# Optimization experiments

Hardware: AMD Instinct MI355X
Metric: run time of the kernel (lower is better)

The kernel has to match this reference:

```python
import jax, jax.numpy as jnp
import numpy as np


def _l2norm(x, eps=1e-12):
    # F.normalize(p=2, dim=-1): x / max(||x||_2, eps)
    n = jnp.linalg.norm(x, axis=-1, keepdims=True)
    return x / jnp.maximum(n, eps)


def _dwconv3x3(x, w):
    # depthwise 3x3 conv, padding=1, no bias. x: [B,C,H,W], w: [C,1,3,3]
    return jax.lax.conv_general_dilated(
        x, w, window_strides=(1, 1), padding='SAME',
        feature_group_count=x.shape[1],
        dimension_numbers=('NCHW', 'OIHW', 'NCHW'))


def setup_inputs() -> dict:
    key = jax.random.key(0)
    ks = jax.random.split(key, 10)
    B, H, W, C = 2, 256, 256, 64
    heads, dh, dim_out = 8, 64, 64
    hd = heads * dh  # 512
    s = 0.02
    return {
        'x_in': jax.random.normal(ks[0], (B, H, W, C), jnp.float32),
        'Wq': jax.random.normal(ks[1], (C, hd), jnp.float32) * s,
        'Wk': jax.random.normal(ks[2], (C, hd), jnp.float32) * s,
        'Wv': jax.random.normal(ks[3], (C, hd), jnp.float32) * s,
        'rescale': jnp.ones((heads, 1, 1), jnp.float32),
        'Wproj': jax.random.normal(ks[4], (hd, dim_out), jnp.float32) * s,
        'bproj': jnp.zeros((dim_out,), jnp.float32),
        'Wc1d': jax.random.normal(ks[5], (hd, dim_out), jnp.float32) * s,
        'bc1d': jnp.zeros((dim_out,), jnp.float32),
        'Wpe1': jax.random.normal(ks[6], (dim_out, 1, 3, 3), jnp.float32) * s,
        'Wpe2': jax.random.normal(ks[7], (dim_out, 1, 3, 3), jnp.float32) * s,
    }


def reference(x_in, Wq, Wk, Wv, rescale, Wproj, bproj, Wc1d, bc1d, Wpe1, Wpe2):
    b, h, w, c = x_in.shape
    heads = rescale.shape[0]
    hd = Wq.shape[1]
    dh = hd // heads
    dim_out = Wproj.shape[1]
    ds = 2

    # AvgPool2d(2,2) on channels-last input
    xp = x_in.reshape(b, h // ds, ds, w // ds, ds, c).mean(axis=(2, 4))
    n_ds = (h // ds) * (w // ds)
    xd = xp.reshape(b, n_ds, c)

    # q,k from downsampled tokens; v from full-res tokens
    q = (xd @ Wq).reshape(b, n_ds, heads, dh).transpose(0, 2, 3, 1)   # [b,heads,dh,n_ds]
    k = (xd @ Wk).reshape(b, n_ds, heads, dh).transpose(0, 2, 3, 1)   # [b,heads,dh,n_ds]
    v_inp = x_in.reshape(b, h * w, c) @ Wv                             # [b,n,hd]
    v = v_inp.reshape(b, h * w, heads, dh).transpose(0, 2, 3, 1)       # [b,heads,dh,n]

    q = _l2norm(q)
    k = _l2norm(k)

    # channel (transposed) attention: [b,heads,dh,dh]
    attn = jnp.einsum('bhin,bhjn->bhij', k, q) * rescale
    attn = jax.nn.softmax(attn, axis=-1)

    xa = jnp.einsum('bhij,bhjn->bhin', attn, v)                        # [b,heads,dh,n]
    xa = xa.transpose(0, 3, 1, 2).reshape(b, h * w, hd)                # [b,n,hd]
    out_c = (xa @ Wproj + bproj).reshape(b, h, w, dim_out)

    # positional branch: 1x1 conv (pointwise) then two depthwise 3x3 convs with GELU
    p = v_inp @ Wc1d + bc1d                                            # [b,n,dim_out]
    p = p.reshape(b, h, w, dim_out).transpose(0, 3, 1, 2)              # [b,dim_out,h,w]
    p = _dwconv3x3(p, Wpe1)
    p = jax.nn.gelu(p, approximate=False)
    p = _dwconv3x3(p, Wpe2)
    out_p = p.transpose(0, 2, 3, 1)                                    # [b,h,w,dim_out]

    return out_c + out_p
```

## Files before the change

### kernel.cpp

```cpp
#include <hip/hip_runtime.h>
#include <math.h>


typedef unsigned short u16;
typedef unsigned int u32;
typedef __attribute__((ext_vector_type(8))) short short8;
typedef __attribute__((ext_vector_type(4))) float f32x4;

__device__ __forceinline__ float bf2f(u16 h) { return __uint_as_float(((u32)h) << 16); }
__device__ __forceinline__ u16 f2bf(float f) {
    u32 u = __float_as_uint(f);
    return (u16)((u + 0x7fffu + ((u >> 16) & 1u)) >> 16);
}
__device__ __forceinline__ float rbf(float f) { return bf2f(f2bf(f)); }
__device__ __forceinline__ u32 pk2(float lo, float hi) {
    return (u32)f2bf(lo) | ((u32)f2bf(hi) << 16);
}
__device__ __forceinline__ void unpack8(uint4 v, float* f) {
    u32 a[4] = {v.x, v.y, v.z, v.w};
#pragma unroll
    for (int i = 0; i < 4; ++i) {
        f[2 * i]     = __uint_as_float(a[i] << 16);
        f[2 * i + 1] = __uint_as_float(a[i] & 0xffff0000u);
    }
}
__device__ __forceinline__ float gelu_exact(float v) {
    return 0.5f * v * (1.f + erff(v * 0.70710678118654752f));
}

__global__ __launch_bounds__(256) void k_front(
    const float* __restrict__ x,
    const float* __restrict__ wq_f, const float* __restrict__ wk_f,
    const float* __restrict__ wv_f, const float* __restrict__ rs_f,
    const float* __restrict__ wp_f, const float* __restrict__ bp_f,
    const float* __restrict__ wc_f, const float* __restrict__ bc_f,
    const float* __restrict__ p1_f, const float* __restrict__ p2_f,
    u32* __restrict__ wb32, float* __restrict__ Wpos,
    u16* __restrict__ xb, float* __restrict__ partials) {
    __shared__ float xvs[64 * 68];
    int blk = blockIdx.x;
    int t = threadIdx.x;
    if (blk < 323) {
        u32 pid = (u32)blk * 256u + t;
        if (pid < 82564u) {
            const float* src; u32 p;
            if      (pid < 16384u) { src = wq_f; p = pid; }
            else if (pid < 32768u) { src = wk_f; p = pid - 16384u; }
            else if (pid < 49152u) { src = wv_f; p = pid - 32768u; }
            else if (pid < 49156u) { src = rs_f; p = pid - 49152u; }
            else if (pid < 65540u) { src = wp_f; p = pid - 49156u; }
            else if (pid < 65572u) { src = bp_f; p = pid - 65540u; }
            else if (pid < 81956u) { src = wc_f; p = pid - 65572u; }
            else if (pid < 81988u) { src = bc_f; p = pid - 81956u; }
            else if (pid < 82276u) { src = p1_f; p = pid - 81988u; }
            else                   { src = p2_f; p = pid - 82276u; }
            wb32[pid] = (u32)f2bf(src[2 * p]) | ((u32)f2bf(src[2 * p + 1]) << 16);
        }
    } else if (blk < 387) {
        int c = blk - 323;
        int o = t & 63, ch = t >> 6;
        const float* wvr = wv_f + c * 512 + ch * 128;
        const float* wcr = wc_f + (size_t)(ch * 128) * 64 + o;
        float s = 0.f;
        for (int kk = 0; kk < 128; ++kk)
            s += rbf(wvr[kk]) * rbf(wcr[(size_t)kk * 64]);
        xvs[ch * 64 + o] = s;
        __syncthreads();
        if (t < 64)
            Wpos[c * 64 + t] = (xvs[t] + xvs[64 + t]) + (xvs[128 + t] + xvs[192 + t]);
    } else {
        int gb = blk - 387;
        int b = gb >> 8, sub = gb & 255;
        int py = sub >> 1, half = sub & 1;
        const size_t rowbase = (size_t)(b * 256 + 2 * py) * 16384 + (size_t)half * 8192;
#pragma unroll
        for (int i2 = 0; i2 < 4; ++i2) {
            int u = t + 256 * i2;
            int P = u >> 4, cq = u & 15;
            size_t o0 = rowbase + (size_t)(2 * P) * 64 + cq * 4;
            float4 a0 = *(const float4*)(x + o0);
            float4 a1 = *(const float4*)(x + o0 + 64);
            float4 a2 = *(const float4*)(x + o0 + 16384);
            float4 a3 = *(const float4*)(x + o0 + 16384 + 64);
            *(uint2*)(xb + o0)              = make_uint2(pk2(a0.x, a0.y), pk2(a0.z, a0.w));
            *(uint2*)(xb + o0 + 64)         = make_uint2(pk2(a1.x, a1.y), pk2(a1.z, a1.w));
            *(uint2*)(xb + o0 + 16384)      = make_uint2(pk2(a2.x, a2.y), pk2(a2.z, a2.w));
            *(uint2*)(xb + o0 + 16384 + 64) = make_uint2(pk2(a3.x, a3.y), pk2(a3.z, a3.w));
            float4 s;
            s.x = 0.25f * (a0.x + a1.x + a2.x + a3.x);
            s.y = 0.25f * (a0.y + a1.y + a2.y + a3.y);
            s.z = 0.25f * (a0.z + a1.z + a2.z + a3.z);
            s.w = 0.25f * (a0.w + a1.w + a2.w + a3.w);
            *(float4*)(&xvs[P * 68 + cq * 4]) = s;
        }
        __syncthreads();
        int r0 = (t >> 4) << 2, c0 = (t & 15) << 2;
        float acc[4][4] = {{0.f}};
        for (int P = 0; P < 64; ++P) {
            float4 av = *(const float4*)(&xvs[P * 68 + r0]);
            float4 bv = *(const float4*)(&xvs[P * 68 + c0]);
            float ar[4] = {av.x, av.y, av.z, av.w};
            float br[4] = {bv.x, bv.y, bv.z, bv.w};
#pragma unroll
            for (int i = 0; i < 4; ++i)
#pragma unroll
                for (int j = 0; j < 4; ++j)
                    acc[i][j] += ar[i] * br[j];
        }
        float* outp = partials + (size_t)gb * 4096;
#pragma unroll
        for (int i = 0; i < 4; ++i)
            *(float4*)(&outp[(r0 + i) * 64 + c0]) =
                make_float4(acc[i][0], acc[i][1], acc[i][2], acc[i][3]);
    }
}

__global__ __launch_bounds__(256) void k_mid1(
    const float* __restrict__ partials, float* __restrict__ G4, float* __restrict__ Weff,
    const u16* __restrict__ xb, const float* __restrict__ Wpos,
    const u16* __restrict__ bc1d, u16* __restrict__ pbuf) {
    __shared__ u16 sm[128 * 72];
    int blk = blockIdx.x;
    int t = threadIdx.x;
    if (blk < 128) {
        int gid = blk * 256 + t;
        int e = gid & 4095, ch = (gid >> 12) & 3, b = gid >> 14;
        const float* p0 = partials + ((size_t)(b * 256 + ch * 64)) * 4096 + e;
        float s = 0.f;
        for (int p = 0; p < 64; ++p)
            s += p0[(size_t)p * 4096];
        G4[gid] = s;
        if (gid < 8192) Weff[gid] = 0.f;
        return;
    }
    int pb = blk - 128;
    int lane = t & 63, wv = t >> 6;
    int col = lane & 15, quad = lane >> 4;

    short8 bf[2][4];
#pragma unroll
    for (int kh = 0; kh < 2; ++kh)
#pragma unroll
        for (int nt = 0; nt < 4; ++nt) {
            short8 v;
#pragma unroll
            for (int j = 0; j < 8; ++j)
                v[j] = (short)f2bf(Wpos[(kh * 32 + quad * 8 + j) * 64 + nt * 16 + col]);
            bf[kh][nt] = v;
        }
    float bias[4];
#pragma unroll
    for (int nt = 0; nt < 4; ++nt) bias[nt] = bf2f(bc1d[nt * 16 + col]);

    size_t base = (size_t)pb * 128;
#pragma unroll
    for (int g = 0; g < 2; ++g) {
        int P0 = wv * 32 + g * 16;
        const short8* ap = (const short8*)(xb + (base + P0 + col) * 64);
        short8 a0 = ap[quad];
        short8 a1 = ap[4 + quad];
#pragma unroll
        for (int nt = 0; nt < 4; ++nt) {
            f32x4 acc = {0.f, 0.f, 0.f, 0.f};
            acc = __builtin_amdgcn_mfma_f32_16x16x32_bf16(a0, bf[0][nt], acc, 0, 0, 0);
            acc = __builtin_amdgcn_mfma_f32_16x16x32_bf16(a1, bf[1][nt], acc, 0, 0, 0);
#pragma unroll
            for (int r = 0; r < 4; ++r)
                sm[(P0 + quad * 4 + r) * 72 + nt * 16 + col] = f2bf(acc[r] + bias[nt]);
        }
    }
    __syncthreads();
#pragma unroll
    for (int k = 0; k < 4; ++k) {
        int linear = k * 256 + t;
        int px = linear >> 3, oct = linear & 7;
        uint4 v = *(const uint4*)(&sm[px * 72 + oct * 8]);
        *(uint4*)(pbuf + (base + px) * 64 + oct * 8) = v;
    }
}

__global__ __launch_bounds__(256) void k_gwqk_norms(
    const float* __restrict__ G4, const u16* __restrict__ wqb, const u16* __restrict__ wkb,
    float* __restrict__ T, float* __restrict__ nq, float* __restrict__ nk) {
    __shared__ __align__(16) float Gs[64 * 68];
    __shared__ __align__(16) float Ps[64 * 68];
    int blk = blockIdx.x, t = threadIdx.x;
    int b = blk >> 4, sel = (blk >> 3) & 1, jg = blk & 7;
    const u16* Wsel = sel ? wkb : wqb;
    {
        int base = t * 16;
        int row = base >> 6, col = base & 63;
        const float* Gb = G4 + (size_t)b * 16384;
#pragma unroll
        for (int q = 0; q < 4; ++q) {
            float4 g0 = *(const float4*)(&Gb[base + 4 * q]);
            float4 g1 = *(const float4*)(&Gb[4096 + base + 4 * q]);
            float4 g2 = *(const float4*)(&Gb[8192 + base + 4 * q]);
            float4 g3 = *(const float4*)(&Gb[12288 + base + 4 * q]);
            *(float4*)(&Gs[row * 68 + col + 4 * q]) = make_float4(
                (g0.x + g1.x) + (g2.x + g3.x), (g0.y + g1.y) + (g2.y + g3.y),
                (g0.z + g1.z) + (g2.z + g3.z), (g0.w + g1.w) + (g2.w + g3.w));
        }
    }
    __syncthreads();
    int c = t >> 2, jq = t & 3;
    int jbase = jg * 64 + jq * 16;
    float Tr[16];
#pragma unroll
    for (int jj = 0; jj < 16; ++jj) Tr[jj] = 0.f;
    for (int k = 0; k < 64; ++k) {
        short8 w0 = *(const short8*)(&Wsel[k * 512 + jbase]);
        short8 w1 = *(const short8*)(&Wsel[k * 512 + jbase + 8]);
        float g = Gs[c * 68 + k];
#pragma unroll
        for (int jj = 0; jj < 8; ++jj) {
            Tr[jj]     += g * bf2f((u16)w0[jj]);
            Tr[8 + jj] += g * bf2f((u16)w1[jj]);
        }
    }
    if (sel == 0) {
#pragma unroll
        for (int q = 0; q < 4; ++q)
            *(float4*)(&T[(size_t)(b * 64 + c) * 512 + jbase + 4 * q]) =
                make_float4(Tr[4 * q], Tr[4 * q + 1], Tr[4 * q + 2], Tr[4 * q + 3]);
    }
    {
        short8 wc0 = *(const short8*)(&Wsel[c * 512 + jbase]);
        short8 wc1 = *(const short8*)(&Wsel[c * 512 + jbase + 8]);
#pragma unroll
        for (int jj = 0; jj < 8; ++jj) {
            Ps[c * 68 + jq * 16 + jj]     = bf2f((u16)wc0[jj]) * Tr[jj];
            Ps[c * 68 + jq * 16 + 8 + jj] = bf2f((u16)wc1[jj]) * Tr[8 + jj];
        }
    }
    __syncthreads();
    if (t < 64) {
        float s = 0.f;
        for (int cc = 0; cc < 64; ++cc) s += Ps[cc * 68 + t];
        float n = fmaxf(sqrtf(fmaxf(s, 0.f)), 1e-12f);
        (sel ? nk : nq)[b * 512 + jg * 64 + t] = n;
    }
}

__global__ __launch_bounds__(256) void k_mid2(
    const u16* __restrict__ wkb, const u16* __restrict__ wpb, const u16* __restrict__ wvb,
    const u16* __restrict__ rsb,
    const float* __restrict__ T, const float* __restrict__ nq, const float* __restrict__ nk,
    float* __restrict__ Weff,
    const u16* __restrict__ pbuf, const u16* __restrict__ wpe1, u16* __restrict__ tbuf) {
    __shared__ __align__(16) char shm[53248];
    int blk = blockIdx.x, t = threadIdx.x;
    if (blk < 16) {
        float* Ts    = (float*)shm;
        float* attns = (float*)(shm + 17408);
        u16*   Wks   = (u16*)(shm + 34816);
        u16*   Wpjs  = (u16*)(shm + 44032);
        float* Pls = Ts;
        u16*   Wvs = Wks;
        int b = blk >> 3, h = blk & 7;
        {
            int c = t >> 2, j0 = (t & 3) * 16;
#pragma unroll
            for (int q = 0; q < 4; ++q)
                *(float4*)(&Ts[c * 68 + j0 + 4 * q]) =
                    *(const float4*)(&T[(size_t)(b * 64 + c) * 512 + h * 64 + j0 + 4 * q]);
            *(short8*)(&Wks[c * 72 + j0])     = *(const short8*)(&wkb[c * 512 + h * 64 + j0]);
            *(short8*)(&Wks[c * 72 + j0 + 8]) = *(const short8*)(&wkb[c * 512 + h * 64 + j0 + 8]);
            *(short8*)(&Wpjs[c * 72 + j0])     = *(const short8*)(&wpb[(h * 64 + c) * 64 + j0]);
            *(short8*)(&Wpjs[c * 72 + j0 + 8]) = *(const short8*)(&wpb[(h * 64 + c) * 64 + j0 + 8]);
        }
        __syncthreads();
        {
            int i = t >> 2, jq = t & 3;
            float L[16];
#pragma unroll
            for (int jj = 0; jj < 16; ++jj) L[jj] = 0.f;
            for (int c = 0; c < 64; ++c) {
                float wk = bf2f(Wks[c * 72 + i]);
#pragma unroll
                for (int q = 0; q < 4; ++q) {
                    float4 tv = *(const float4*)(&Ts[c * 68 + jq * 16 + 4 * q]);
                    L[4 * q + 0] += wk * tv.x;
                    L[4 * q + 1] += wk * tv.y;
                    L[4 * q + 2] += wk * tv.z;
                    L[4 * q + 3] += wk * tv.w;
                }
            }
            float rs = bf2f(rsb[h]);
            float nki = nk[b * 512 + h * 64 + i];
            float nqv[16];
#pragma unroll
            for (int q = 0; q < 4; ++q) {
                float4 nv = *(const float4*)(&nq[b * 512 + h * 64 + jq * 16 + 4 * q]);
                nqv[4 * q] = nv.x; nqv[4 * q + 1] = nv.y;
                nqv[4 * q + 2] = nv.z; nqv[4 * q + 3] = nv.w;
            }
            float m = -1e30f;
#pragma unroll
            for (int jj = 0; jj < 16; ++jj) {
                L[jj] = L[jj] * rs / (nki * nqv[jj]);
                m = fmaxf(m, L[jj]);
            }
            m = fmaxf(m, __shfl_xor(m, 1));
            m = fmaxf(m, __shfl_xor(m, 2));
            float s = 0.f;
#pragma unroll
            for (int jj = 0; jj < 16; ++jj) {
                L[jj] = __expf(L[jj] - m);
                s += L[jj];
            }
            s += __shfl_xor(s, 1);
            s += __shfl_xor(s, 2);
            float inv = 1.f / s;
#pragma unroll
            for (int q = 0; q < 4; ++q)
                *(float4*)(&attns[i * 68 + jq * 16 + 4 * q]) =
                    make_float4(L[4 * q] * inv, L[4 * q + 1] * inv,
                                L[4 * q + 2] * inv, L[4 * q + 3] * inv);
        }
        __syncthreads();
        {
            int c = t >> 2, j0 = (t & 3) * 16;
            *(short8*)(&Wvs[c * 72 + j0])     = *(const short8*)(&wvb[c * 512 + h * 64 + j0]);
            *(short8*)(&Wvs[c * 72 + j0 + 8]) = *(const short8*)(&wvb[c * 512 + h * 64 + j0 + 8]);
            int j = t >> 2, oq = t & 3;
            float Pl[16];
#pragma unroll
            for (int jj = 0; jj < 16; ++jj) Pl[jj] = 0.f;
            for (int i2 = 0; i2 < 64; ++i2) {
                float a = attns[i2 * 68 + j];
                short8 w0 = *(const short8*)(&Wpjs[i2 * 72 + oq * 16]);
                short8 w1 = *(const short8*)(&Wpjs[i2 * 72 + oq * 16 + 8]);
#pragma unroll
                for (int jj = 0; jj < 8; ++jj) {
                    Pl[jj]     += a * bf2f((u16)w0[jj]);
                    Pl[8 + jj] += a * bf2f((u16)w1[jj]);
                }
            }
#pragma unroll
            for (int q = 0; q < 4; ++q)
                *(float4*)(&Pls[j * 68 + oq * 16 + 4 * q]) =
                    make_float4(Pl[4 * q], Pl[4 * q + 1], Pl[4 * q + 2], Pl[4 * q + 3]);
        }
        __syncthreads();
        {
            int c = t >> 2, oq = t & 3;
            float acc[16];
#pragma unroll
            for (int jj = 0; jj < 16; ++jj) acc[jj] = 0.f;
            for (int j2 = 0; j2 < 64; ++j2) {
                float wv = bf2f(Wvs[c * 72 + j2]);
#pragma unroll
                for (int q = 0; q < 4; ++q) {
                    float4 pv = *(const float4*)(&Pls[j2 * 68 + oq * 16 + 4 * q]);
                    acc[4 * q + 0] += wv * pv.x;
                    acc[4 * q + 1] += wv * pv.y;
                    acc[4 * q + 2] += wv * pv.z;
                    acc[4 * q + 3] += wv * pv.w;
                }
            }
            float* W = Weff + b * 4096 + c * 64 + oq * 16;
#pragma unroll
            for (int jj = 0; jj < 16; ++jj) atomicAdd(&W[jj], acc[jj]);
        }
        return;
    }
    u16* sm = (u16*)shm;
    int cb = blk - 16;
    int b  = cb >> 9;
    int ty = (cb >> 3) & 63;
    int tx = cb & 7;
    int gy0 = ty * 4, gx0 = tx * 32;

    for (int i = t; i < 1632; i += 256) {
        int px = i >> 3, ch = i & 7;
        int hy = px / 34, hx = px - hy * 34;
        int gy = gy0 + hy - 1, gx = gx0 + hx - 1;
        uint4 v = make_uint4(0, 0, 0, 0);
        if ((unsigned)gy < 256u && (unsigned)gx < 256u)
            v = *(const uint4*)(pbuf + ((size_t)((b << 16) + (gy << 8) + gx)) * 64 + ch * 8);
        *(uint4*)(&sm[px * 72 + ch * 8]) = v;
    }
    int oct = t & 7;
    float w[8][9];
#pragma unroll
    for (int j = 0; j < 8; ++j)
#pragma unroll
        for (int k = 0; k < 9; ++k) w[j][k] = bf2f(wpe1[(oct * 8 + j) * 9 + k]);
    __syncthreads();

#pragma unroll
    for (int s = 0; s < 4; ++s) {
        int lp = (t >> 3) + s * 32;
        int ly = lp >> 5, lx = lp & 31;
        float acc[8] = {0.f, 0.f, 0.f, 0.f, 0.f, 0.f, 0.f, 0.f};
#pragma unroll
        for (int dy = 0; dy < 3; ++dy)
#pragma unroll
            for (int dx = 0; dx < 3; ++dx) {
                int hp = (ly + dy) * 34 + lx + dx;
                uint4 v = *(const uint4*)(&sm[hp * 72 + oct * 8]);
                float f[8];
                unpack8(v, f);
                int tap = dy * 3 + dx;
#pragma unroll
                for (int j = 0; j < 8; ++j) acc[j] += f[j] * w[j][tap];
            }
        u32 pk[4];
#pragma unroll
        for (int q = 0; q < 4; ++q)
            pk[q] = pk2(gelu_exact(acc[2 * q]), gelu_exact(acc[2 * q + 1]));
        size_t gpix = (size_t)(b << 16) + ((size_t)(gy0 + ly) << 8) + gx0 + lx;
        *(uint4*)(tbuf + gpix * 64 + oct * 8) = make_uint4(pk[0], pk[1], pk[2], pk[3]);
    }
}

__global__ __launch_bounds__(256) void k_final(const u16* __restrict__ xb,
                                               const u16* __restrict__ tbuf,
                                               const float* __restrict__ Weff,
                                               const u16* __restrict__ wpe2,
                                               const u16* __restrict__ bproj,
                                               float* __restrict__ out) {
    __shared__ u16 sm[204 * 72];
    __shared__ float stage[128 * 68];
    int t = threadIdx.x;
    int blk = blockIdx.x;
    int b  = blk >> 9;
    int ty = (blk >> 3) & 63;
    int tx = blk & 7;
    int gy0 = ty * 4, gx0 = tx * 32;

    for (int i = t; i < 1632; i += 256) {
        int px = i >> 3, ch = i & 7;
        int hy = px / 34, hx = px - hy * 34;
        int gy = gy0 + hy - 1, gx = gx0 + hx - 1;
        uint4 v = make_uint4(0, 0, 0, 0);
        if ((unsigned)gy < 256u && (unsigned)gx < 256u)
            v = *(const uint4*)(tbuf + ((size_t)((b << 16) + (gy << 8) + gx)) * 64 + ch * 8);
        *(uint4*)(&sm[px * 72 + ch * 8]) = v;
    }
    int oct = t & 7;
    {
        float w[8][9];
#pragma unroll
        for (int j = 0; j < 8; ++j)
#pragma unroll
            for (int k = 0; k < 9; ++k) w[j][k] = bf2f(wpe2[(oct * 8 + j) * 9 + k]);
        __syncthreads();
#pragma unroll
        for (int s = 0; s < 4; ++s) {
            int lp = (t >> 3) + s * 32;
            int ly = lp >> 5, lx = lp & 31;
            float acc[8] = {0.f, 0.f, 0.f, 0.f, 0.f, 0.f, 0.f, 0.f};
#pragma unroll
            for (int dy = 0; dy < 3; ++dy)
#pragma unroll
                for (int dx = 0; dx < 3; ++dx) {
                    int hp = (ly + dy) * 34 + lx + dx;
                    uint4 v = *(const uint4*)(&sm[hp * 72 + oct * 8]);
                    float f[8];
                    unpack8(v, f);
                    int tap = dy * 3 + dx;
#pragma unroll
                    for (int j = 0; j < 8; ++j) acc[j] += f[j] * w[j][tap];
                }
#pragma unroll
            for (int j = 0; j < 8; ++j)
                stage[lp * 68 + oct * 8 + j] = acc[j];
        }
    }
    __syncthreads();

    int lane = t & 63, wv = t >> 6;
    int col = lane & 15, quad = lane >> 4;
    const float* W = Weff + b * 4096;
    short8 bf[2][4];
#pragma unroll
    for (int kh = 0; kh < 2; ++kh)
#pragma unroll
        for (int nt = 0; nt < 4; ++nt) {
            short8 v;
#pragma unroll
            for (int j = 0; j < 8; ++j)
                v[j] = (short)f2bf(W[(kh * 32 + quad * 8 + j) * 64 + nt * 16 + col]);
            bf[kh][nt] = v;
        }
    float bias[4];
#pragma unroll
    for (int nt = 0; nt < 4; ++nt) bias[nt] = bf2f(bproj[nt * 16 + col]);

#pragma unroll
    for (int g = 0; g < 2; ++g) {
        int grp = wv * 2 + g;
        int ly = grp >> 1;
        int lxb = (grp & 1) * 16;
        size_t rowpix = (size_t)(b << 16) + ((size_t)(gy0 + ly) << 8) + gx0;
        const short8* ap = (const short8*)(xb + (rowpix + lxb + col) * 64);
        short8 a0 = ap[quad];
        short8 a1 = ap[4 + quad];
#pragma unroll
        for (int nt = 0; nt < 4; ++nt) {
            f32x4 acc = {0.f, 0.f, 0.f, 0.f};
            acc = __builtin_amdgcn_mfma_f32_16x16x32_bf16(a0, bf[0][nt], acc, 0, 0, 0);
            acc = __builtin_amdgcn_mfma_f32_16x16x32_bf16(a1, bf[1][nt], acc, 0, 0, 0);
#pragma unroll
            for (int r = 0; r < 4; ++r) {
                int lp = ly * 32 + lxb + quad * 4 + r;
                stage[lp * 68 + nt * 16 + col] += acc[r] + bias[nt];
            }
        }
    }
    __syncthreads();

#pragma unroll
    for (int k = 0; k < 8; ++k) {
        int linear = k * 256 + t;
        int px = linear >> 4, c4 = linear & 15;
        int ly = px >> 5, lx = px & 31;
        float4 v = *(const float4*)(&stage[px * 68 + c4 * 4]);
        size_t gpix = (size_t)(b << 16) + ((size_t)(gy0 + ly) << 8) + gx0 + lx;
        *(float4*)(out + gpix * 64 + c4 * 4) = v;
    }
}

extern "C" void kernel_launch(void* const* d_in, const int* in_sizes, int n_in,
                              void* d_out, int out_size, void* d_ws, size_t ws_size,
                              hipStream_t stream) {
    const float* x = (const float*)d_in[0];
    float* out = (float*)d_out;

    char* w = (char*)d_ws;
    size_t off = 0;
    auto alloc = [&](size_t bytes) -> void* {
        void* p = w + off;
        off += (bytes + 255) & ~(size_t)255;
        return p;
    };
    u16* xb = (u16*)alloc((size_t)16777216 * 2);
    u16* wb = (u16*)alloc((size_t)165128 * 2);
    u16* wqb = wb;
    u16* wkb = wqb + 32768;
    u16* wvb = wkb + 32768;
    u16* rsb = wvb + 32768;
    u16* wpb = rsb + 8;
    u16* bpb = wpb + 32768;
    u16* wcb = bpb + 64;
    u16* bcb = wcb + 32768;
    u16* p1b = bcb + 64;
    u16* p2b = p1b + 576;
    (void)wcb;

    float* partials = (float*)alloc((size_t)512 * 4096 * 4);
    float* G4       = (float*)alloc((size_t)2 * 4 * 4096 * 4);
    float* T        = (float*)alloc((size_t)2 * 64 * 512 * 4);
    float* nq       = (float*)alloc((size_t)2 * 512 * 4);
    float* nk       = (float*)alloc((size_t)2 * 512 * 4);
    float* Weff     = (float*)alloc((size_t)2 * 4096 * 4);
    float* Wpos     = (float*)alloc((size_t)4096 * 4);
    u16*   pbuf     = (u16*)alloc((size_t)2 * 65536 * 64 * 2);
    u16*   tbuf     = (u16*)alloc((size_t)2 * 65536 * 64 * 2);

    hipLaunchKernelGGL(k_front, dim3(899), dim3(256), 0, stream,
                       x,
                       (const float*)d_in[1], (const float*)d_in[2], (const float*)d_in[3],
                       (const float*)d_in[4], (const float*)d_in[5], (const float*)d_in[6],
                       (const float*)d_in[7], (const float*)d_in[8], (const float*)d_in[9],
                       (const float*)d_in[10],
                       (u32*)wb, Wpos, xb, partials);
    hipLaunchKernelGGL(k_mid1, dim3(1152), dim3(256), 0, stream,
                       partials, G4, Weff, xb, Wpos, bcb, pbuf);
    hipLaunchKernelGGL(k_gwqk_norms, dim3(32), dim3(256), 0, stream,
                       G4, wqb, wkb, T, nq, nk);
    hipLaunchKernelGGL(k_mid2, dim3(1040), dim3(256), 0, stream,
                       wkb, wpb, wvb, rsb, T, nq, nk, Weff, pbuf, p1b, tbuf);
    hipLaunchKernelGGL(k_final, dim3(1024), dim3(256), 0, stream,
                       xb, tbuf, Weff, p2b, bpb, out);
}
```

Before: 166.9 us.

## Fuse Gram-weight product and norm kernel into attention mid-stage blocks

Removes the separate k_gwqk_norms launch and computes the G·Wq/G·Wk products and the q/k norms directly inside the 16 attention blocks of k_mid2, keeping T and the norms in shared memory rather than in global buffers. This saves one kernel launch and a global round-trip for T, nq and nk. In exchange each attention block does more serial work: two 64x64x64 products plus reductions with extra barriers, and Wk is now read from global memory inside the logits loop instead of from shared memory. That lengthens the critical path of the 16 heavy blocks that run alongside the conv blocks.

New measurement: 174.0 us. +4.3%, slower.

```diff
diff --git a/kernel.cpp b/kernel.cpp
--- a/kernel.cpp
+++ b/kernel.cpp
@@ -179,107 +179,115 @@
     }
 }
 
-__global__ __launch_bounds__(256) void k_gwqk_norms(
-    const float* __restrict__ G4, const u16* __restrict__ wqb, const u16* __restrict__ wkb,
-    float* __restrict__ T, float* __restrict__ nq, float* __restrict__ nk) {
-    __shared__ __align__(16) float Gs[64 * 68];
-    __shared__ __align__(16) float Ps[64 * 68];
-    int blk = blockIdx.x, t = threadIdx.x;
-    int b = blk >> 4, sel = (blk >> 3) & 1, jg = blk & 7;
-    const u16* Wsel = sel ? wkb : wqb;
-    {
-        int base = t * 16;
-        int row = base >> 6, col = base & 63;
-        const float* Gb = G4 + (size_t)b * 16384;
-#pragma unroll
-        for (int q = 0; q < 4; ++q) {
-            float4 g0 = *(const float4*)(&Gb[base + 4 * q]);
-            float4 g1 = *(const float4*)(&Gb[4096 + base + 4 * q]);
-            float4 g2 = *(const float4*)(&Gb[8192 + base + 4 * q]);
-            float4 g3 = *(const float4*)(&Gb[12288 + base + 4 * q]);
-            *(float4*)(&Gs[row * 68 + col + 4 * q]) = make_float4(
-                (g0.x + g1.x) + (g2.x + g3.x), (g0.y + g1.y) + (g2.y + g3.y),
-                (g0.z + g1.z) + (g2.z + g3.z), (g0.w + g1.w) + (g2.w + g3.w));
-        }
-    }
-    __syncthreads();
-    int c = t >> 2, jq = t & 3;
-    int jbase = jg * 64 + jq * 16;
-    float Tr[16];
-#pragma unroll
-    for (int jj = 0; jj < 16; ++jj) Tr[jj] = 0.f;
-    for (int k = 0; k < 64; ++k) {
-        short8 w0 = *(const short8*)(&Wsel[k * 512 + jbase]);
-        short8 w1 = *(const short8*)(&Wsel[k * 512 + jbase + 8]);
-        float g = Gs[c * 68 + k];
-#pragma unroll
-        for (int jj = 0; jj < 8; ++jj) {
-            Tr[jj]     += g * bf2f((u16)w0[jj]);
-            Tr[8 + jj] += g * bf2f((u16)w1[jj]);
-        }
-    }
-    if (sel == 0) {
-#pragma unroll
-        for (int q = 0; q < 4; ++q)
-            *(float4*)(&T[(size_t)(b * 64 + c) * 512 + jbase + 4 * q]) =
-                make_float4(Tr[4 * q], Tr[4 * q + 1], Tr[4 * q + 2], Tr[4 * q + 3]);
-    }
-    {
-        short8 wc0 = *(const short8*)(&Wsel[c * 512 + jbase]);
-        short8 wc1 = *(const short8*)(&Wsel[c * 512 + jbase + 8]);
-#pragma unroll
-        for (int jj = 0; jj < 8; ++jj) {
-            Ps[c * 68 + jq * 16 + jj]     = bf2f((u16)wc0[jj]) * Tr[jj];
-            Ps[c * 68 + jq * 16 + 8 + jj] = bf2f((u16)wc1[jj]) * Tr[8 + jj];
-        }
-    }
-    __syncthreads();
-    if (t < 64) {
-        float s = 0.f;
-        for (int cc = 0; cc < 64; ++cc) s += Ps[cc * 68 + t];
-        float n = fmaxf(sqrtf(fmaxf(s, 0.f)), 1e-12f);
-        (sel ? nk : nq)[b * 512 + jg * 64 + t] = n;
-    }
-}
-
 __global__ __launch_bounds__(256) void k_mid2(
-    const u16* __restrict__ wkb, const u16* __restrict__ wpb, const u16* __restrict__ wvb,
+    const u16* __restrict__ wkb, const u16* __restrict__ wqb,
+    const u16* __restrict__ wpb, const u16* __restrict__ wvb,
     const u16* __restrict__ rsb,
-    const float* __restrict__ T, const float* __restrict__ nq, const float* __restrict__ nk,
-    float* __restrict__ Weff,
+    const float* __restrict__ G4, float* __restrict__ Weff,
     const u16* __restrict__ pbuf, const u16* __restrict__ wpe1, u16* __restrict__ tbuf) {
     __shared__ __align__(16) char shm[53248];
     int blk = blockIdx.x, t = threadIdx.x;
     if (blk < 16) {
-        float* Ts    = (float*)shm;
-        float* attns = (float*)(shm + 17408);
-        u16*   Wks   = (u16*)(shm + 34816);
-        u16*   Wpjs  = (u16*)(shm + 44032);
-        float* Pls = Ts;
-        u16*   Wvs = Wks;
+        float* Ts   = (float*)shm;
+        float* Ps   = (float*)(shm + 17408);
+        float* Gs   = (float*)(shm + 34816);
+        u16*   Wpjs = (u16*)(shm + 34816);
+        u16*   Wvs  = (u16*)(shm + 34816 + 9216);
+        float* attns = Ps;
+        float* Pls   = Ts;
         int b = blk >> 3, h = blk & 7;
-        {
-            int c = t >> 2, j0 = (t & 3) * 16;
+        int c = t >> 2, jq = t & 3, j0 = jq * 16;
+        {
+            int base = t * 16;
+            int row = base >> 6, col = base & 63;
+            const float* Gb = G4 + (size_t)b * 16384;
+#pragma unroll
+            for (int q = 0; q < 4; ++q) {
+                float4 g0 = *(const float4*)(&Gb[base + 4 * q]);
+                float4 g1 = *(const float4*)(&Gb[4096 + base + 4 * q]);
+                float4 g2 = *(const float4*)(&Gb[8192 + base + 4 * q]);
+                float4 g3 = *(const float4*)(&Gb[12288 + base + 4 * q]);
+                *(float4*)(&Gs[row * 68 + col + 4 * q]) = make_float4(
+                    (g0.x + g1.x) + (g2.x + g3.x), (g0.y + g1.y) + (g2.y + g3.y),
+                    (g0.z + g1.z) + (g2.z + g3.z), (g0.w + g1.w) + (g2.w + g3.w));
+            }
+        }
+        __syncthreads();
+        float Tr[16];
+        {
+#pragma unroll
+            for (int jj = 0; jj < 16; ++jj) Tr[jj] = 0.f;
+            for (int k = 0; k < 64; ++k) {
+                short8 w0 = *(const short8*)(&wkb[k * 512 + h * 64 + j0]);
+                short8 w1 = *(const short8*)(&wkb[k * 512 + h * 64 + j0 + 8]);
+                float g = Gs[c * 68 + k];
+#pragma unroll
+                for (int jj = 0; jj < 8; ++jj) {
+                    Tr[jj]     += g * bf2f((u16)w0[jj]);
+                    Tr[8 + jj] += g * bf2f((u16)w1[jj]);
+                }
+            }
+            short8 wc0 = *(const short8*)(&wkb[c * 512 + h * 64 + j0]);
+            short8 wc1 = *(const short8*)(&wkb[c * 512 + h * 64 + j0 + 8]);
+#pragma unroll
+            for (int jj = 0; jj < 8; ++jj) {
+                Ps[c * 68 + j0 + jj]     = bf2f((u16)wc0[jj]) * Tr[jj];
+                Ps[c * 68 + j0 + 8 + jj] = bf2f((u16)wc1[jj]) * Tr[8 + jj];
+            }
+        }
+        __syncthreads();
+        if (t < 64) {
+            float s = 0.f;
+            for (int cc = 0; cc < 64; ++cc) s += Ps[cc * 68 + t];
+            Ts[t * 68 + 64] = fmaxf(sqrtf(fmaxf(s, 0.f)), 1e-12f);
+        }
+        {
+#pragma unroll
+            for (int jj = 0; jj < 16; ++jj) Tr[jj] = 0.f;
+            for (int k = 0; k < 64; ++k) {
+                short8 w0 = *(const short8*)(&wqb[k * 512 + h * 64 + j0]);
+                short8 w1 = *(const short8*)(&wqb[k * 512 + h * 64 + j0 + 8]);
+                float g = Gs[c * 68 + k];
+#pragma unroll
+                for (int jj = 0; jj < 8; ++jj) {
+                    Tr[jj]     += g * bf2f((u16)w0[jj]);
+                    Tr[8 + jj] += g * bf2f((u16)w1[jj]);
+                }
+            }
 #pragma unroll
             for (int q = 0; q < 4; ++q)
                 *(float4*)(&Ts[c * 68 + j0 + 4 * q]) =
-                    *(const float4*)(&T[(size_t)(b * 64 + c) * 512 + h * 64 + j0 + 4 * q]);
-            *(short8*)(&Wks[c * 72 + j0])     = *(const short8*)(&wkb[c * 512 + h * 64 + j0]);
-            *(short8*)(&Wks[c * 72 + j0 + 8]) = *(const short8*)(&wkb[c * 512 + h * 64 + j0 + 8]);
+                    make_float4(Tr[4 * q], Tr[4 * q + 1], Tr[4 * q + 2], Tr[4 * q + 3]);
+        }
+        __syncthreads();
+        {
+            short8 wc0 = *(const short8*)(&wqb[c * 512 + h * 64 + j0]);
+            short8 wc1 = *(const short8*)(&wqb[c * 512 + h * 64 + j0 + 8]);
+#pragma unroll
+            for (int jj = 0; jj < 8; ++jj) {
+                Ps[c * 68 + j0 + jj]     = bf2f((u16)wc0[jj]) * Tr[jj];
+                Ps[c * 68 + j0 + 8 + jj] = bf2f((u16)wc1[jj]) * Tr[8 + jj];
+            }
             *(short8*)(&Wpjs[c * 72 + j0])     = *(const short8*)(&wpb[(h * 64 + c) * 64 + j0]);
             *(short8*)(&Wpjs[c * 72 + j0 + 8]) = *(const short8*)(&wpb[(h * 64 + c) * 64 + j0 + 8]);
         }
         __syncthreads();
-        {
-            int i = t >> 2, jq = t & 3;
+        if (t < 64) {
+            float s = 0.f;
+            for (int cc = 0; cc < 64; ++cc) s += Ps[cc * 68 + t];
+            Ts[t * 68 + 65] = fmaxf(sqrtf(fmaxf(s, 0.f)), 1e-12f);
+        }
+        __syncthreads();
+        {
+            int i = t >> 2;
             float L[16];
 #pragma unroll
             for (int jj = 0; jj < 16; ++jj) L[jj] = 0.f;
-            for (int c = 0; c < 64; ++c) {
-                float wk = bf2f(Wks[c * 72 + i]);
+            for (int c2 = 0; c2 < 64; ++c2) {
+                float wk = bf2f(wkb[c2 * 512 + h * 64 + i]);
 #pragma unroll
                 for (int q = 0; q < 4; ++q) {
-                    float4 tv = *(const float4*)(&Ts[c * 68 + jq * 16 + 4 * q]);
+                    float4 tv = *(const float4*)(&Ts[c2 * 68 + j0 + 4 * q]);
                     L[4 * q + 0] += wk * tv.x;
                     L[4 * q + 1] += wk * tv.y;
                     L[4 * q + 2] += wk * tv.z;
@@ -287,14 +295,10 @@
                 }
             }
             float rs = bf2f(rsb[h]);
-            float nki = nk[b * 512 + h * 64 + i];
+            float nki = Ts[i * 68 + 64];
             float nqv[16];
 #pragma unroll
-            for (int q = 0; q < 4; ++q) {
-                float4 nv = *(const float4*)(&nq[b * 512 + h * 64 + jq * 16 + 4 * q]);
-                nqv[4 * q] = nv.x; nqv[4 * q + 1] = nv.y;
-                nqv[4 * q + 2] = nv.z; nqv[4 * q + 3] = nv.w;
-            }
+            for (int jj = 0; jj < 16; ++jj) nqv[jj] = Ts[(j0 + jj) * 68 + 65];
             float m = -1e30f;
 #pragma unroll
             for (int jj = 0; jj < 16; ++jj) {
@@ -314,13 +318,12 @@
             float inv = 1.f / s;
 #pragma unroll
             for (int q = 0; q < 4; ++q)
-                *(float4*)(&attns[i * 68 + jq * 16 + 4 * q]) =
+                *(float4*)(&attns[i * 68 + j0 + 4 * q]) =
                     make_float4(L[4 * q] * inv, L[4 * q + 1] * inv,
                                 L[4 * q + 2] * inv, L[4 * q + 3] * inv);
         }
         __syncthreads();
         {
-            int c = t >> 2, j0 = (t & 3) * 16;
             *(short8*)(&Wvs[c * 72 + j0])     = *(const short8*)(&wvb[c * 512 + h * 64 + j0]);
             *(short8*)(&Wvs[c * 72 + j0 + 8]) = *(const short8*)(&wvb[c * 512 + h * 64 + j0 + 8]);
             int j = t >> 2, oq = t & 3;
@@ -344,7 +347,7 @@
         }
         __syncthreads();
         {
-            int c = t >> 2, oq = t & 3;
+            int oq = t & 3;
             float acc[16];
 #pragma unroll
             for (int jj = 0; jj < 16; ++jj) acc[jj] = 0.f;
@@ -552,9 +555,6 @@
 
     float* partials = (float*)alloc((size_t)512 * 4096 * 4);
     float* G4       = (float*)alloc((size_t)2 * 4 * 4096 * 4);
-    float* T        = (float*)alloc((size_t)2 * 64 * 512 * 4);
-    float* nq       = (float*)alloc((size_t)2 * 512 * 4);
-    float* nk       = (float*)alloc((size_t)2 * 512 * 4);
     float* Weff     = (float*)alloc((size_t)2 * 4096 * 4);
     float* Wpos     = (float*)alloc((size_t)4096 * 4);
     u16*   pbuf     = (u16*)alloc((size_t)2 * 65536 * 64 * 2);
@@ -569,10 +569,8 @@
                        (u32*)wb, Wpos, xb, partials);
     hipLaunchKernelGGL(k_mid1, dim3(1152), dim3(256), 0, stream,
                        partials, G4, Weff, xb, Wpos, bcb, pbuf);
-    hipLaunchKernelGGL(k_gwqk_norms, dim3(32), dim3(256), 0, stream,
-                       G4, wqb, wkb, T, nq, nk);
     hipLaunchKernelGGL(k_mid2, dim3(1040), dim3(256), 0, stream,
-                       wkb, wpb, wvb, rsb, T, nq, nk, Weff, pbuf, p1b, tbuf);
+                       wkb, wqb, wpb, wvb, rsb, G4, Weff, pbuf, p1b, tbuf);
     hipLaunchKernelGGL(k_final, dim3(1024), dim3(256), 0, stream,
                        xb, tbuf, Weff, p2b, bpb, out);
 }
```
